# Kernel optimization log

Hardware: AMD Instinct MI355X
Metric: run time of the kernel (lower is better)

The kernel has to match this reference:

```python
import jax, jax.numpy as jnp
import numpy as np

BLOCK_LEN = 128
NUM_HEADS = 16


def setup_inputs() -> dict:
    key = jax.random.key(0)
    k0, k1, k2 = jax.random.split(key, 3)
    D = 1024
    x = jax.random.normal(k0, (2, 8192, D), dtype=jnp.float32)
    Wqkv = jax.random.normal(k1, (D, 3 * D), dtype=jnp.float32) * 0.02
    bqkv = jnp.zeros((3 * D,), dtype=jnp.float32)
    Wout = jax.random.normal(k2, (D, D), dtype=jnp.float32) * 0.02
    bout = jnp.zeros((D,), dtype=jnp.float32)
    return {"x": x, "Wqkv": Wqkv, "bqkv": bqkv, "Wout": Wout, "bout": bout}


def reference(x, Wqkv, bqkv, Wout, bout):
    B, S, D = x.shape
    H = NUM_HEADS
    BL = BLOCK_LEN
    NB = S // BL            # number of blocks (rows)
    HD = D // H             # head dim (qkv_ratio=1.0 -> qkv_dim_total == D)

    qkv = x @ Wqkv + bqkv                                   # [B, S, 3D]
    qkv = qkv.reshape(B, NB, BL, 3, H, HD)
    q = qkv[:, :, :, 0]                                     # [B, NB, BL, H, HD]
    k = qkv[:, :, :, 1]
    v = qkv[:, :, :, 2]

    # 'column' attention: attend across blocks at the same within-block position.
    # permute to [B, BL(pos p), H, NB(block n), HD]
    qc = jnp.transpose(q, (0, 2, 3, 1, 4))
    kc = jnp.transpose(k, (0, 2, 3, 1, 4))
    vc = jnp.transpose(v, (0, 2, 3, 1, 4))

    scale = 1.0 / jnp.sqrt(jnp.asarray(HD, dtype=x.dtype))
    scores = jnp.einsum('bphnd,bphmd->bphnm', qc, kc) * scale   # [B,BL,H,NB,NB]
    causal = jnp.tril(jnp.ones((NB, NB), dtype=bool))
    scores = jnp.where(causal, scores, jnp.asarray(-1e9, dtype=scores.dtype))
    w = jax.nn.softmax(scores, axis=-1)
    o = jnp.einsum('bphnm,bphmd->bphnd', w, vc)                 # [B,BL,H,NB,HD]

    # back to [B, NB, BL, H*HD] -> [B, S, D]
    o = jnp.transpose(o, (0, 3, 1, 2, 4)).reshape(B, S, D)
    return o @ Wout + bout
```

## Files before the change

### kernel.cpp

```cpp
#include <hip/hip_runtime.h>
#include <stdint.h>

typedef unsigned short u16;
typedef __attribute__((ext_vector_type(8))) short s16x8;
typedef __attribute__((ext_vector_type(4))) float f32x4;

__device__ __forceinline__ f32x4 mfma16x16(s16x8 a, s16x8 b, f32x4 c) {
    return __builtin_amdgcn_mfma_f32_16x16x32_bf16(a, b, c, 0, 0, 0);
}

__device__ __forceinline__ u16 f2bf(float f) {
    union { float f; unsigned u; } c; c.f = f;
    unsigned u = c.u;
    return (u16)((u + 0x7FFFu + ((u >> 16) & 1u)) >> 16);
}

__device__ __forceinline__ void gload16(const void* g, void* l) {
    auto gp = (const __attribute__((address_space(1))) unsigned int*)(g);
    auto lp = (__attribute__((address_space(3))) unsigned int*)(l);
    __builtin_amdgcn_global_load_lds(gp, lp, 16, 0, 0);
}

__device__ __forceinline__ void wave_sync() {
    __builtin_amdgcn_sched_barrier(0);
    asm volatile("s_waitcnt vmcnt(0) lgkmcnt(0)" ::: "memory");
    __builtin_amdgcn_sched_barrier(0);
    __builtin_amdgcn_s_barrier();
    __builtin_amdgcn_sched_barrier(0);
}

__global__ __launch_bounds__(256) void convert_x(
    const float* __restrict__ src, u16* __restrict__ dst, long n)
{
    const long stride = (long)gridDim.x * 256 * 8;
    for (long i = ((long)blockIdx.x * 256 + threadIdx.x) * 8; i < n; i += stride) {
        const float4 a = *(const float4*)(src + i);
        const float4 b = *(const float4*)(src + i + 4);
        u16 o[8] = { f2bf(a.x), f2bf(a.y), f2bf(a.z), f2bf(a.w),
                     f2bf(b.x), f2bf(b.y), f2bf(b.z), f2bf(b.w) };
        *(s16x8*)(dst + i) = *(const s16x8*)o;
    }
}

__global__ __launch_bounds__(256) void fill_sentinel(float* __restrict__ o, long n)
{
    const long stride = (long)gridDim.x * 256;
    for (long i = (long)blockIdx.x * 256 + threadIdx.x; i < n; i += stride)
        o[i] = 1.0f;
}

__global__ __launch_bounds__(256) void transpose_f32_bf16(
    const float* __restrict__ in, u16* __restrict__ out, int R, int C)
{
    __shared__ u16 t[32][33];
    const int c0 = blockIdx.x * 32, r0 = blockIdx.y * 32;
    const int tx = threadIdx.x & 31, ty = threadIdx.x >> 5;
#pragma unroll
    for (int i = 0; i < 32; i += 8)
        t[ty + i][tx] = f2bf(in[(long)(r0 + ty + i) * C + c0 + tx]);
    __syncthreads();
#pragma unroll
    for (int i = 0; i < 32; i += 8)
        out[(long)(c0 + ty + i) * R + r0 + tx] = t[tx][ty + i];
}

template <int FP32OUT, int NT, int NBN>
__global__ __launch_bounds__(512, 2) void gemm256(
    const u16* __restrict__ A, const u16* __restrict__ BT,
    const float* __restrict__ bias, void* __restrict__ Cout,
    int N, int K)
{
    extern __shared__ char smem[];
    char* const As = smem;
    char* const Bs = smem + 65536;

    const int tid  = threadIdx.x;
    const int lane = tid & 63;
    const int wid  = tid >> 6;
    const int rr   = lane & 15, g = lane >> 4;
    const int wr   = wid >> 2;
    const int wc   = wid & 3;

    const int nwg = gridDim.x;
    const int gsw = ((int)blockIdx.x & 7) * (nwg >> 3) + ((int)blockIdx.x >> 3);
    const long m0 = (long)(gsw / NBN) * 256;
    const long n0 = (long)(gsw % NBN) * 256;

    const int cl = (tid & 3) ^ ((tid >> 3) & 3);
    const u16* pA0 = A  + (m0 + (tid >> 2)) * (long)K + cl * 8;
    const u16* pA1 = pA0 + 128 * (long)K;
    const u16* pB0 = BT + (n0 + (tid >> 2)) * (long)K + cl * 8;
    const u16* pB1 = pB0 + 128 * (long)K;
    const int sdst = wid * 1024;

    const int xg   = (g ^ ((rr >> 1) & 3)) << 4;
    const int arow = (wr * 128 + rr) * 64 + xg;
    const int brow = (wc * 64  + rr) * 64 + xg;

#define STA(tt, h) { const long c_ = (long)(tt) * 64 + (h) * 32;              \
        char* d_ = As + (((tt) & 1) * 2 + (h)) * 16384 + sdst;                \
        gload16(pA0 + c_, d_); gload16(pA1 + c_, d_ + 8192); }
#define STB(tt, h) { const long c_ = (long)(tt) * 64 + (h) * 32;              \
        char* d_ = Bs + (((tt) & 1) * 2 + (h)) * 16384 + sdst;                \
        gload16(pB0 + c_, d_); gload16(pB1 + c_, d_ + 8192); }
#define SB() __builtin_amdgcn_sched_barrier(0)
#define RD(Bf, Af, half, bufsel)                                              \
    { _Pragma("unroll") for (int n_ = 0; n_ < 4; ++n_)                        \
          Bf[n_] = *(const s16x8*)(Bs + (bufsel) + (half) + brow + n_ * 1024);\
      _Pragma("unroll") for (int m_ = 0; m_ < 8; ++m_)                        \
          Af[m_] = *(const s16x8*)(As + (bufsel) + (half) + arow + m_ * 1024);}
#define MM(Af, Bf)                                                            \
    { SB(); __builtin_amdgcn_s_setprio(1);                                    \
      _Pragma("unroll") for (int m_ = 0; m_ < 8; ++m_)                        \
      _Pragma("unroll") for (int n_ = 0; n_ < 4; ++n_)                        \
          acc[m_][n_] = mfma16x16(Af[m_], Bf[n_], acc[m_][n_]);               \
      __builtin_amdgcn_s_setprio(0); SB(); }

    f32x4 acc[8][4] = {};
    s16x8 B0[4], A0[8], B1[4], A1[8];

    STA(0, 0); STB(0, 0); STA(0, 1); STB(0, 1); STA(1, 0); STB(1, 0);
    asm volatile("s_waitcnt vmcnt(4)" ::: "memory");
    SB(); __builtin_amdgcn_s_barrier(); SB();
    RD(B0, A0, 0, 0);

    for (int t = 0; t < NT; ++t) {
        const int ab = (t & 1) * 32768;
        const int nb = ((t + 1) & 1) * 32768;

        if (t > 0) {
            if (t == NT - 1) { asm volatile("s_waitcnt vmcnt(0)" ::: "memory"); }
            else             { asm volatile("s_waitcnt vmcnt(4)" ::: "memory"); }
            SB(); __builtin_amdgcn_s_barrier(); SB();
        }
        RD(B1, A1, 16384, ab);
        SB();
        if (t + 1 < NT) { STA(t + 1, 1); STB(t + 1, 1); }
        MM(A0, B0);

        if (t < NT - 1) {
            asm volatile("s_waitcnt vmcnt(4)" ::: "memory");
            SB(); __builtin_amdgcn_s_barrier(); SB();
            RD(B0, A0, 0, nb);
            SB();
            if (t + 2 < NT) { STA(t + 2, 0); STB(t + 2, 0); }
        }
        MM(A1, B1);
    }
#undef STA
#undef STB
#undef SB
#undef RD
#undef MM

    float bv[4];
#pragma unroll
    for (int n = 0; n < 4; ++n)
        bv[n] = bias[n0 + wc * 64 + n * 16 + rr];
#pragma unroll
    for (int m = 0; m < 8; ++m) {
        const long rb = m0 + wr * 128 + m * 16 + g * 4;
#pragma unroll
        for (int r = 0; r < 4; ++r) {
            const long rowoff = (rb + r) * N + n0 + wc * 64 + rr;
#pragma unroll
            for (int n = 0; n < 4; ++n) {
                const float v = acc[m][n][r] + bv[n];
                if (FP32OUT) ((float*)Cout)[rowoff + n * 16] = v;
                else         ((u16*)Cout)[rowoff + n * 16] = f2bf(v);
            }
        }
    }
}

__global__ __launch_bounds__(64) void attn_blocks(
    const u16* __restrict__ qkv, u16* __restrict__ o)
{
    __shared__ u16 Vlds[64 * 64];
    __shared__ u16 Plds[64 * 72];
    const int bid = blockIdx.x;
    const int b = bid >> 11;
    const int h = (bid >> 7) & 15;
    const int p = bid & 127;
    const int lane = threadIdx.x;
    const int rr = lane & 15, g = lane >> 4;
    const long NSTR = 128L * 3072;
    const long base = ((long)b * 8192 + p) * 3072 + h * 64;

    {
        const int vrow = lane >> 3;
        const int vchunk = (lane & 7) ^ (vrow & 7);
#pragma unroll
        for (int q = 0; q < 8; ++q)
            gload16(qkv + base + (long)(q * 8 + vrow) * NSTR + 2048 + vchunk * 8,
                    (char*)Vlds + q * 1024);
    }

    s16x8 kf[4][2], qf[4][2];
#pragma unroll
    for (int t = 0; t < 4; ++t)
#pragma unroll
        for (int ks = 0; ks < 2; ++ks) {
            const long roff = base + (long)(t * 16 + rr) * NSTR + ks * 32 + g * 8;
            kf[t][ks] = *(const s16x8*)(qkv + roff + 1024);
            qf[t][ks] = *(const s16x8*)(qkv + roff);
        }

    f32x4 T[4][4] = {};
#pragma unroll
    for (int ks = 0; ks < 2; ++ks)
#pragma unroll
        for (int i = 0; i < 4; ++i)
#pragma unroll
            for (int jn = 0; jn < 4; ++jn)
                T[i][jn] = mfma16x16(kf[i][ks], qf[jn][ks], T[i][jn]);

    const float scale = 0.125f;
#pragma unroll
    for (int jn = 0; jn < 4; ++jn) {
        const int n = jn * 16 + rr;
        float pv[16];
        float mx = -3e38f;
#pragma unroll
        for (int i = 0; i < 4; ++i)
#pragma unroll
            for (int r = 0; r < 4; ++r) {
                const int m = i * 16 + g * 4 + r;
                const float s = (m <= n) ? T[i][jn][r] * scale : -3e38f;
                pv[i * 4 + r] = s;
                mx = fmaxf(mx, s);
            }
        mx = fmaxf(mx, __shfl_xor(mx, 16));
        mx = fmaxf(mx, __shfl_xor(mx, 32));
        float sum = 0.f;
#pragma unroll
        for (int t = 0; t < 16; ++t) {
            const float e = (pv[t] > -1e30f) ? __expf(pv[t] - mx) : 0.f;
            pv[t] = e;
            sum += e;
        }
        sum += __shfl_xor(sum, 16);
        sum += __shfl_xor(sum, 32);
        const float inv = 1.f / sum;
#pragma unroll
        for (int i = 0; i < 4; ++i)
#pragma unroll
            for (int rp = 0; rp < 2; ++rp) {
                const int m = i * 16 + g * 4 + rp * 2;
                const unsigned lo = f2bf(pv[i * 4 + rp * 2] * inv);
                const unsigned hi = f2bf(pv[i * 4 + rp * 2 + 1] * inv);
                *(unsigned*)((char*)Plds + n * 144 + m * 2) = lo | (hi << 16);
            }
    }

    wave_sync();

    f32x4 O[4][4] = {};
#pragma unroll
    for (int ks = 0; ks < 2; ++ks) {
        s16x8 pa[4];
#pragma unroll
        for (int in = 0; in < 4; ++in)
            pa[in] = *(const s16x8*)((const char*)Plds +
                      (in * 16 + rr) * 144 + ks * 64 + g * 16);
#pragma unroll
        for (int jd = 0; jd < 4; ++jd) {
            s16x8 vb;
#pragma unroll
            for (int j = 0; j < 8; ++j) {
                const int k = ks * 32 + g * 8 + j;
                const int byte = (k * 128 + (jd * 16 + rr) * 2) ^ ((k & 7) << 4);
                vb[j] = *(const short*)((const char*)Vlds + byte);
            }
#pragma unroll
            for (int in = 0; in < 4; ++in)
                O[in][jd] = mfma16x16(pa[in], vb, O[in][jd]);
        }
    }

    const long obase = ((long)b * 8192 + p) * 1024 + h * 64;
#pragma unroll
    for (int in = 0; in < 4; ++in)
#pragma unroll
        for (int r = 0; r < 4; ++r) {
            const long n = in * 16 + g * 4 + r;
#pragma unroll
            for (int jd = 0; jd < 4; ++jd) {
                const long d = jd * 16 + rr;
                o[obase + n * (128L * 1024) + d] = f2bf(O[in][jd][r]);
            }
        }
}

extern "C" void kernel_launch(void* const* d_in, const int* in_sizes, int n_in,
                              void* d_out, int out_size, void* d_ws, size_t ws_size,
                              hipStream_t stream) {
    const float* x    = (const float*)d_in[0];
    const float* Wqkv = (const float*)d_in[1];
    const float* bq   = (const float*)d_in[2];
    const float* Wout = (const float*)d_in[3];
    const float* bo   = (const float*)d_in[4];

    char* ws = (char*)d_ws;
    u16* xb    = (u16*)(ws);
    u16* qkv   = (u16*)(ws +  33554432L);
    u16* ob    = (u16*)(ws + 134217728L);
    u16* WqkvT = (u16*)(ws + 167772160L);
    u16* WoutT = (u16*)(ws + 174063616L);
    const size_t NEEDED = 176160768UL;

    if (ws_size < NEEDED) {
        fill_sentinel<<<2048, 256, 0, stream>>>((float*)d_out, (long)out_size);
        return;
    }

    (void)hipFuncSetAttribute(reinterpret_cast<const void*>(&gemm256<0, 16, 12>),
                              hipFuncAttributeMaxDynamicSharedMemorySize, 131072);
    (void)hipFuncSetAttribute(reinterpret_cast<const void*>(&gemm256<1, 16, 4>),
                              hipFuncAttributeMaxDynamicSharedMemorySize, 131072);

    convert_x<<<2048, 256, 0, stream>>>(x, xb, 16777216L);
    transpose_f32_bf16<<<dim3(96, 32), 256, 0, stream>>>(Wqkv, WqkvT, 1024, 3072);
    transpose_f32_bf16<<<dim3(32, 32), 256, 0, stream>>>(Wout, WoutT, 1024, 1024);

    gemm256<0, 16, 12><<<768, 512, 131072, stream>>>(xb, WqkvT, bq, qkv,
                                                     3072, 1024);

    attn_blocks<<<4096, 64, 0, stream>>>(qkv, ob);

    gemm256<1, 16, 4><<<256, 512, 131072, stream>>>(ob, WoutT, bo, d_out,
                                                    1024, 1024);
}
```

Measured before the change: 210.8 us.

## Restructure GEMM main loop: full-tile prefetch with interleaved LDS reads and MFMAs

Replaces the staggered half-tile double-buffered main loop with a scheme that issues all global-to-LDS loads for the next K tile at the start of each iteration. The LDS fragment reads for the current tile are split into quarter chunks and interleaved with MFMA groups of 4x4. This cuts to one barrier per iteration and shrinks the live register fragments, which may help occupancy or scheduling. In exchange, prefetch depth drops to a single tile, and it waits for all outstanding loads (vmcnt(0)) before each barrier, so it may hide less global latency.

Measured after the change: 196.6 us. -6.7%, faster.

```diff
diff --git a/kernel.cpp b/kernel.cpp
--- a/kernel.cpp
+++ b/kernel.cpp
@@ -104,53 +104,60 @@
         char* d_ = Bs + (((tt) & 1) * 2 + (h)) * 16384 + sdst;                \
         gload16(pB0 + c_, d_); gload16(pB1 + c_, d_ + 8192); }
 #define SB() __builtin_amdgcn_sched_barrier(0)
-#define RD(Bf, Af, half, bufsel)                                              \
-    { _Pragma("unroll") for (int n_ = 0; n_ < 4; ++n_)                        \
-          Bf[n_] = *(const s16x8*)(Bs + (bufsel) + (half) + brow + n_ * 1024);\
-      _Pragma("unroll") for (int m_ = 0; m_ < 8; ++m_)                        \
-          Af[m_] = *(const s16x8*)(As + (bufsel) + (half) + arow + m_ * 1024);}
-#define MM(Af, Bf)                                                            \
+#define MM(Af, Bf, mb)                                                        \
     { SB(); __builtin_amdgcn_s_setprio(1);                                    \
-      _Pragma("unroll") for (int m_ = 0; m_ < 8; ++m_)                        \
+      _Pragma("unroll") for (int m_ = 0; m_ < 4; ++m_)                        \
       _Pragma("unroll") for (int n_ = 0; n_ < 4; ++n_)                        \
-          acc[m_][n_] = mfma16x16(Af[m_], Bf[n_], acc[m_][n_]);               \
+          acc[(mb) + m_][n_] = mfma16x16(Af[m_], Bf[n_], acc[(mb) + m_][n_]); \
       __builtin_amdgcn_s_setprio(0); SB(); }
 
     f32x4 acc[8][4] = {};
-    s16x8 B0[4], A0[8], B1[4], A1[8];
-
-    STA(0, 0); STB(0, 0); STA(0, 1); STB(0, 1); STA(1, 0); STB(1, 0);
-    asm volatile("s_waitcnt vmcnt(4)" ::: "memory");
+
+    STA(0, 0); STB(0, 0); STA(0, 1); STB(0, 1);
+    asm volatile("s_waitcnt vmcnt(0)" ::: "memory");
     SB(); __builtin_amdgcn_s_barrier(); SB();
-    RD(B0, A0, 0, 0);
 
     for (int t = 0; t < NT; ++t) {
         const int ab = (t & 1) * 32768;
-        const int nb = ((t + 1) & 1) * 32768;
-
-        if (t > 0) {
-            if (t == NT - 1) { asm volatile("s_waitcnt vmcnt(0)" ::: "memory"); }
-            else             { asm volatile("s_waitcnt vmcnt(4)" ::: "memory"); }
+        s16x8 fB0[4], fA0[4], fA1[4], fB1[4], fA2[4], fA3[4];
+
+        if (t + 1 < NT) { STA(t + 1, 0); STB(t + 1, 0);
+                          STA(t + 1, 1); STB(t + 1, 1); }
+        SB();
+
+#pragma unroll
+        for (int n = 0; n < 4; ++n)
+            fB0[n] = *(const s16x8*)(Bs + ab + brow + n * 1024);
+#pragma unroll
+        for (int m = 0; m < 4; ++m)
+            fA0[m] = *(const s16x8*)(As + ab + arow + m * 1024);
+#pragma unroll
+        for (int m = 0; m < 4; ++m)
+            fA1[m] = *(const s16x8*)(As + ab + arow + (m + 4) * 1024);
+        MM(fA0, fB0, 0);
+
+#pragma unroll
+        for (int n = 0; n < 4; ++n)
+            fB1[n] = *(const s16x8*)(Bs + ab + 16384 + brow + n * 1024);
+#pragma unroll
+        for (int m = 0; m < 4; ++m)
+            fA2[m] = *(const s16x8*)(As + ab + 16384 + arow + m * 1024);
+        MM(fA1, fB0, 4);
+
+#pragma unroll
+        for (int m = 0; m < 4; ++m)
+            fA3[m] = *(const s16x8*)(As + ab + 16384 + arow + (m + 4) * 1024);
+        MM(fA2, fB1, 0);
+        MM(fA3, fB1, 4);
+
+        if (t < NT - 1) {
+            asm volatile("s_waitcnt vmcnt(0)" ::: "memory");
             SB(); __builtin_amdgcn_s_barrier(); SB();
         }
-        RD(B1, A1, 16384, ab);
-        SB();
-        if (t + 1 < NT) { STA(t + 1, 1); STB(t + 1, 1); }
-        MM(A0, B0);
-
-        if (t < NT - 1) {
-            asm volatile("s_waitcnt vmcnt(4)" ::: "memory");
-            SB(); __builtin_amdgcn_s_barrier(); SB();
-            RD(B0, A0, 0, nb);
-            SB();
-            if (t + 2 < NT) { STA(t + 2, 0); STB(t + 2, 0); }
-        }
-        MM(A1, B1);
     }
 #undef STA
 #undef STB
 #undef SB
-#undef RD
 #undef MM
 
     float bv[4];
```

## Load GEMM B fragments directly from global into registers, halve LDS

Applied to the files above, without the earlier changes.

The GEMM no longer stages the B (weight) tile through LDS. Each wave loads its B fragments straight from global memory into registers, while A stays double-buffered in LDS. This halves shared memory per block to 64KB and removes the B LDS reads, but each of the two waves sharing a column block now fetches B from global separately. B is no longer shared through LDS, which raises global/L2 traffic and exposes vector-load latency inside the pipeline.

Measured after the change: 280.2 us. 32.9% more time.

```diff
diff --git a/kernel.cpp b/kernel.cpp
--- a/kernel.cpp
+++ b/kernel.cpp
@@ -72,7 +72,6 @@
 {
     extern __shared__ char smem[];
     char* const As = smem;
-    char* const Bs = smem + 65536;
 
     const int tid  = threadIdx.x;
     const int lane = tid & 63;
@@ -87,70 +86,79 @@
     const long n0 = (long)(gsw % NBN) * 256;
 
     const int cl = (tid & 3) ^ ((tid >> 3) & 3);
-    const u16* pA0 = A  + (m0 + (tid >> 2)) * (long)K + cl * 8;
+    const u16* pA0 = A + (m0 + (tid >> 2)) * (long)K + cl * 8;
     const u16* pA1 = pA0 + 128 * (long)K;
-    const u16* pB0 = BT + (n0 + (tid >> 2)) * (long)K + cl * 8;
-    const u16* pB1 = pB0 + 128 * (long)K;
     const int sdst = wid * 1024;
 
     const int xg   = (g ^ ((rr >> 1) & 3)) << 4;
     const int arow = (wr * 128 + rr) * 64 + xg;
-    const int brow = (wc * 64  + rr) * 64 + xg;
+
+    const u16* pBr = BT + (n0 + wc * 64 + rr) * (long)K + g * 8;
 
 #define STA(tt, h) { const long c_ = (long)(tt) * 64 + (h) * 32;              \
         char* d_ = As + (((tt) & 1) * 2 + (h)) * 16384 + sdst;                \
         gload16(pA0 + c_, d_); gload16(pA1 + c_, d_ + 8192); }
-#define STB(tt, h) { const long c_ = (long)(tt) * 64 + (h) * 32;              \
-        char* d_ = Bs + (((tt) & 1) * 2 + (h)) * 16384 + sdst;                \
-        gload16(pB0 + c_, d_); gload16(pB1 + c_, d_ + 8192); }
+#define LDB(dst, tt, kk) { _Pragma("unroll") for (int n_ = 0; n_ < 4; ++n_)   \
+        dst[n_] = *(const s16x8*)(pBr + (long)n_ * 16 * K +                   \
+                                  (long)(tt) * 64 + (kk) * 32); }
 #define SB() __builtin_amdgcn_sched_barrier(0)
-#define RD(Bf, Af, half, bufsel)                                              \
-    { _Pragma("unroll") for (int n_ = 0; n_ < 4; ++n_)                        \
-          Bf[n_] = *(const s16x8*)(Bs + (bufsel) + (half) + brow + n_ * 1024);\
-      _Pragma("unroll") for (int m_ = 0; m_ < 8; ++m_)                        \
-          Af[m_] = *(const s16x8*)(As + (bufsel) + (half) + arow + m_ * 1024);}
-#define MM(Af, Bf)                                                            \
+#define RDA(fX, fY, half, bufsel)                                             \
+    { _Pragma("unroll") for (int m_ = 0; m_ < 4; ++m_)                        \
+          fX[m_] = *(const s16x8*)(As + (bufsel) + (half) + arow + m_ * 1024);\
+      _Pragma("unroll") for (int m_ = 0; m_ < 4; ++m_)                        \
+          fY[m_] = *(const s16x8*)(As + (bufsel) + (half) + arow +            \
+                                   (m_ + 4) * 1024); }
+#define MM(Af, Bf, mb)                                                        \
     { SB(); __builtin_amdgcn_s_setprio(1);                                    \
-      _Pragma("unroll") for (int m_ = 0; m_ < 8; ++m_)                        \
+      _Pragma("unroll") for (int m_ = 0; m_ < 4; ++m_)                        \
       _Pragma("unroll") for (int n_ = 0; n_ < 4; ++n_)                        \
-          acc[m_][n_] = mfma16x16(Af[m_], Bf[n_], acc[m_][n_]);               \
+          acc[(mb) + m_][n_] = mfma16x16(Af[m_], Bf[n_], acc[(mb) + m_][n_]); \
       __builtin_amdgcn_s_setprio(0); SB(); }
 
     f32x4 acc[8][4] = {};
-    s16x8 B0[4], A0[8], B1[4], A1[8];
-
-    STA(0, 0); STB(0, 0); STA(0, 1); STB(0, 1); STA(1, 0); STB(1, 0);
-    asm volatile("s_waitcnt vmcnt(4)" ::: "memory");
+    s16x8 fA0[4], fA1[4], fA2[4], fA3[4];
+    s16x8 B0[4], B1[4];
+
+    STA(0, 0); STA(0, 1); STA(1, 0);
+    LDB(B0, 0, 0);
+    asm volatile("s_waitcnt vmcnt(6)" ::: "memory");
     SB(); __builtin_amdgcn_s_barrier(); SB();
-    RD(B0, A0, 0, 0);
+    RDA(fA0, fA1, 0, 0);
 
     for (int t = 0; t < NT; ++t) {
         const int ab = (t & 1) * 32768;
         const int nb = ((t + 1) & 1) * 32768;
 
         if (t > 0) {
-            if (t == NT - 1) { asm volatile("s_waitcnt vmcnt(0)" ::: "memory"); }
-            else             { asm volatile("s_waitcnt vmcnt(4)" ::: "memory"); }
+            if (t >= NT - 2) { asm volatile("s_waitcnt vmcnt(0)" ::: "memory"); }
+            else             { asm volatile("s_waitcnt vmcnt(6)" ::: "memory"); }
             SB(); __builtin_amdgcn_s_barrier(); SB();
         }
-        RD(B1, A1, 16384, ab);
+        RDA(fA2, fA3, 16384, ab);
         SB();
-        if (t + 1 < NT) { STA(t + 1, 1); STB(t + 1, 1); }
-        MM(A0, B0);
+        if (t + 1 < NT) STA(t + 1, 1);
+        LDB(B1, t, 1);
+        SB();
+        MM(fA0, B0, 0);
+        MM(fA1, B0, 4);
 
         if (t < NT - 1) {
-            asm volatile("s_waitcnt vmcnt(4)" ::: "memory");
+            if (t >= NT - 2) { asm volatile("s_waitcnt vmcnt(0)" ::: "memory"); }
+            else             { asm volatile("s_waitcnt vmcnt(6)" ::: "memory"); }
             SB(); __builtin_amdgcn_s_barrier(); SB();
-            RD(B0, A0, 0, nb);
+            RDA(fA0, fA1, 0, nb);
             SB();
-            if (t + 2 < NT) { STA(t + 2, 0); STB(t + 2, 0); }
-        }
-        MM(A1, B1);
+            if (t + 2 < NT) STA(t + 2, 0);
+            LDB(B0, t + 1, 0);
+            SB();
+        }
+        MM(fA2, B1, 0);
+        MM(fA3, B1, 4);
     }
 #undef STA
-#undef STB
+#undef LDB
 #undef SB
-#undef RD
+#undef RDA
 #undef MM
 
     float bv[4];
@@ -315,19 +323,19 @@
     }
 
     (void)hipFuncSetAttribute(reinterpret_cast<const void*>(&gemm256<0, 16, 12>),
-                              hipFuncAttributeMaxDynamicSharedMemorySize, 131072);
+                              hipFuncAttributeMaxDynamicSharedMemorySize, 65536);
     (void)hipFuncSetAttribute(reinterpret_cast<const void*>(&gemm256<1, 16, 4>),
-                              hipFuncAttributeMaxDynamicSharedMemorySize, 131072);
+                              hipFuncAttributeMaxDynamicSharedMemorySize, 65536);
 
     convert_x<<<2048, 256, 0, stream>>>(x, xb, 16777216L);
     transpose_f32_bf16<<<dim3(96, 32), 256, 0, stream>>>(Wqkv, WqkvT, 1024, 3072);
     transpose_f32_bf16<<<dim3(32, 32), 256, 0, stream>>>(Wout, WoutT, 1024, 1024);
 
-    gemm256<0, 16, 12><<<768, 512, 131072, stream>>>(xb, WqkvT, bq, qkv,
-                                                     3072, 1024);
+    gemm256<0, 16, 12><<<768, 512, 65536, stream>>>(xb, WqkvT, bq, qkv,
+                                                    3072, 1024);
 
     attn_blocks<<<4096, 64, 0, stream>>>(qkv, ob);
 
-    gemm256<1, 16, 4><<<256, 512, 131072, stream>>>(ob, WoutT, bo, d_out,
-                                                    1024, 1024);
-}
+    gemm256<1, 16, 4><<<256, 512, 65536, stream>>>(ob, WoutT, bo, d_out,
+                                                   1024, 1024);
+}
```
